# Kernel optimization log

Hardware: AMD Instinct MI355X
Metric: run time of the kernel (lower is better)

The kernel has to match this reference:

```python
import jax, jax.numpy as jnp
import numpy as np

MUL_IN = 32      # multiplicity of input 0e irrep (input channels)
MUL_OUT = 32     # multiplicity of each output irrep
NUM_RB = 8       # num_radial_basis
DIAMETER = 5.0
STEPS = (1.0, 1.0, 1.0)
GRID = 32
BATCH = 2
OUT_DIM = MUL_OUT * (1 + 3 + 5)  # 32x0e + 32x1o + 32x2e = 288


def _sus(x):
    # smooth unit step used by e3nn's 'smooth_finite' basis
    return jnp.where(x > 0.0, jnp.exp(-1.0 / jnp.where(x > 0.0, x, 1.0)), 0.0)


def _soft_one_hot(x, start, end, number):
    # e3nn.soft_one_hot_linspace, basis='smooth_finite', start_zero=end_zero=True
    values = jnp.linspace(start, end, number + 2)
    step = values[1] - values[0]
    values = values[1:-1]
    d = (x[..., None] - values) / step
    return 1.14136 * jnp.exp(2.0) * _sus(d + 1.0) * _sus(1.0 - d)


def _lattice():
    r = DIAMETER / 2
    axes = []
    for st in STEPS:
        s = int(np.floor(r / st))
        axes.append(jnp.arange(-s, s + 1.0, dtype=jnp.float32) * st)
    return jnp.stack(jnp.meshgrid(*axes, indexing='ij'), axis=-1)  # [X,Y,Z,3]


def _sph(lattice):
    # e3nn real spherical harmonics (component normalization, normalize=True),
    # e3nn axis/order convention: l=1 -> (y, z, x)
    n = jnp.linalg.norm(lattice, axis=-1, keepdims=True)
    u = lattice / jnp.where(n == 0.0, 1.0, n)
    x, y, z = u[..., 0], u[..., 1], u[..., 2]
    y0 = jnp.ones_like(x)[..., None]
    y1 = jnp.sqrt(3.0) * jnp.stack([y, z, x], axis=-1)
    y2 = jnp.stack([
        jnp.sqrt(15.0) * x * y,
        jnp.sqrt(15.0) * y * z,
        (jnp.sqrt(5.0) / 2.0) * (2.0 * z**2 - x**2 - y**2),
        jnp.sqrt(15.0) * x * z,
        (jnp.sqrt(15.0) / 2.0) * (x**2 - y**2),
    ], axis=-1)
    return [y0, y1, y2]


def _kernel(w0, w1, w2, w_lin):
    lat = _lattice()
    nvox = lat.shape[0] * lat.shape[1] * lat.shape[2]
    emb = _soft_one_hot(jnp.linalg.norm(lat, axis=-1), 0.0, DIAMETER / 2, NUM_RB)
    ys = _sph(lat)
    fan = jnp.sqrt(jnp.asarray(MUL_IN, emb.dtype))  # fully-connected TP path norm
    blocks = []
    for w, y in zip((w0, w1, w2), ys):
        # radial weights per (in-mul u, out-mul v): [X,Y,Z,u,v]
        W = jnp.einsum('xyzk,kuv->xyzuv', emb, w) / nvox
        # scalar-input TP path 0e x l -> l reduces to outer product with Y_lm
        blk = jnp.einsum('xyzuv,xyzm->xyzuvm', W, y) / fan
        blocks.append(blk.reshape(blk.shape[:4] + (-1,)))  # flatten (v, m)
    k = jnp.concatenate(blocks, axis=-1)  # [X,Y,Z,MUL_IN,OUT_DIM]
    # self-connection (FunctionalLinear) replaces the center tap; only 0e->0e path
    center = jnp.concatenate(
        [w_lin / fan, jnp.zeros((MUL_IN, MUL_OUT * (3 + 5)), k.dtype)], axis=-1)
    cx, cy, cz = k.shape[0] // 2, k.shape[1] // 2, k.shape[2] // 2
    return k.at[cx, cy, cz].set(center)


def setup_inputs() -> dict:
    key = jax.random.key(0)
    ks = jax.random.split(key, 5)
    return {
        'x': jax.random.normal(ks[0], (BATCH, GRID, GRID, GRID, MUL_IN), jnp.float32),
        'w0': jax.random.normal(ks[1], (NUM_RB, MUL_IN, MUL_OUT), jnp.float32),
        'w1': jax.random.normal(ks[2], (NUM_RB, MUL_IN, MUL_OUT), jnp.float32),
        'w2': jax.random.normal(ks[3], (NUM_RB, MUL_IN, MUL_OUT), jnp.float32),
        'w_lin': jax.random.normal(ks[4], (MUL_IN, MUL_OUT), jnp.float32),
    }


def reference(x, w0, w1, w2, w_lin):
    k = _kernel(w0, w1, w2, w_lin)  # [5,5,5,32,288]
    return jax.lax.conv_general_dilated(
        x, k, window_strides=(1, 1, 1), padding='SAME',
        dimension_numbers=('NXYZC', 'XYZIO', 'NXYZC'))
```

## Files before the change

### kernel.cpp

```cpp
#include <hip/hip_runtime.h>

typedef __bf16 bf16x8 __attribute__((ext_vector_type(8)));
typedef float f32x4 __attribute__((ext_vector_type(4)));

#define KT_BYTES 2304000
#define NS 18432

__device__ __forceinline__ unsigned short f2bf(float f) {
    unsigned int u = __builtin_bit_cast(unsigned int, f);
    unsigned int r = (u + 0x7fffu + ((u >> 16) & 1u)) >> 16;
    return (unsigned short)r;
}

__device__ __forceinline__ float sus(float x) {
    return x > 0.0f ? expf(-1.0f / x) : 0.0f;
}

struct VoxTab { int kt[81]; int xb[81]; };
constexpr VoxTab mk_tab() {
    VoxTab t{};
    int n = 0;
    for (int dx = 0; dx < 5; dx++)
        for (int dy = 0; dy < 5; dy++)
            for (int dz = 0; dz < 5; dz++) {
                int a = dx - 2, b = dy - 2, c = dz - 2;
                if (a * a + b * b + c * c <= 6) {
                    t.kt[n] = (dx * 25 + dy * 5 + dz) * NS;
                    t.xb[n] = ((dx * 36 + dy) * 36 + dz) * 32;
                    n++;
                }
            }
    return t;
}
__constant__ VoxTab TAB = mk_tab();

__global__ __launch_bounds__(512) void build_kt(const float* __restrict__ w0,
                                                const float* __restrict__ w1,
                                                const float* __restrict__ w2,
                                                const float* __restrict__ wlin,
                                                unsigned short* __restrict__ kt) {
    __shared__ float lw[24576];
    const int tid = threadIdx.x;
    {
        const float4* s0 = (const float4*)w0;
        const float4* s1 = (const float4*)w1;
        const float4* s2 = (const float4*)w2;
        for (int u = tid; u < 6144; u += 512) {
            int wsel = u >> 11, r = u & 2047;
            float4 v = (wsel == 0 ? s0[r] : (wsel == 1 ? s1[r] : s2[r]));
            ((float4*)lw)[u] = v;
        }
    }
    __syncthreads();

    const int v = blockIdx.x;
    const int dx = v / 25, dy = (v / 5) % 5, dz = v % 5;
    const float lx = (float)(dx - 2), ly = (float)(dy - 2), lz = (float)(dz - 2);
    const float nr = sqrtf(lx * lx + ly * ly + lz * lz);

    float emb[8];
    const float tt = nr * (9.0f / 2.5f);
    const float C = 1.14136f * expf(2.0f);
    #pragma unroll
    for (int j = 1; j <= 8; j++) {
        float d = tt - (float)j;
        emb[j - 1] = C * sus(d + 1.0f) * sus(1.0f - d);
    }

    float ux = 0.f, uy = 0.f, uz = 0.f;
    if (nr > 0.0f) { ux = lx / nr; uy = ly / nr; uz = lz / nr; }
    float Y[9];
    const float s3 = 1.7320508075688772f, s15 = 3.872983346207417f;
    Y[0] = 1.0f;
    Y[1] = s3 * uy; Y[2] = s3 * uz; Y[3] = s3 * ux;
    Y[4] = s15 * ux * uy;
    Y[5] = s15 * uy * uz;
    Y[6] = 1.1180339887498949f * (2.0f * uz * uz - ux * ux - uy * uy);
    Y[7] = s15 * ux * uz;
    Y[8] = 0.5f * s15 * (ux * ux - uy * uy);

    const float rfan = 0.17677669529663687f;

    for (int e = tid; e < 9216; e += 512) {
        const int ci = e / 288, o = e % 288;
        int wsel, co, yi;
        if (o < 32)       { wsel = 0; co = o; yi = 0; }
        else if (o < 128) { int t = o - 32;  wsel = 1; co = t / 3; yi = 1 + t % 3; }
        else              { int t = o - 128; wsel = 2; co = t / 5; yi = 4 + t % 5; }
        const float* w = lw + wsel * 8192;
        float s = 0.0f;
        #pragma unroll
        for (int k = 0; k < 8; k++) s += emb[k] * w[k * 1024 + ci * 32 + co];
        float val = s * (1.0f / 125.0f) * Y[yi] * rfan;
        if (v == 62) val = (o < 32) ? wlin[ci * 32 + o] * rfan : 0.0f;
        int r = o * 64 + ci * 2;
        int rs = r ^ (((r >> 7) & 7) << 4);
        kt[v * 9216 + (rs >> 1)] = f2bf(val);
    }
}

__global__ void pad_x2(const float* __restrict__ x, unsigned short* __restrict__ xb) {
    int u = blockIdx.x * blockDim.x + threadIdx.x;
    if (u >= 373248) return;
    const int ci8 = u & 3;
    int t = u >> 2;
    const int pz = t % 36; t /= 36;
    const int py = t % 36; t /= 36;
    const int px = t % 36; const int nn = t / 36;
    const int gx = px - 2, gy = py - 2, gz = pz - 2;
    uint4 ov = {0u, 0u, 0u, 0u};
    if ((unsigned)gx < 32u && (unsigned)gy < 32u && (unsigned)gz < 32u) {
        const float* src = x + ((((size_t)nn * 32 + gx) * 32 + gy) * 32 + gz) * 32 + ci8 * 8;
        float4 f0 = ((const float4*)src)[0];
        float4 f1 = ((const float4*)src)[1];
        ov.x = (unsigned)f2bf(f0.x) | ((unsigned)f2bf(f0.y) << 16);
        ov.y = (unsigned)f2bf(f0.z) | ((unsigned)f2bf(f0.w) << 16);
        ov.z = (unsigned)f2bf(f1.x) | ((unsigned)f2bf(f1.y) << 16);
        ov.w = (unsigned)f2bf(f1.z) | ((unsigned)f2bf(f1.w) << 16);
    }
    ((uint4*)xb)[u] = ov;
}

__global__ __launch_bounds__(512, 2) void conv_mfma(const unsigned short* __restrict__ xb,
                                                    const unsigned short* __restrict__ kt,
                                                    float* __restrict__ out) {
    __shared__ __align__(16) char lds[3 * NS];
    const int tid = threadIdx.x;
    const int lane = tid & 63;
    const int wv = tid >> 6;
    const int l15 = lane & 15, l16 = lane >> 4;
    const int wm = wv & 3, wn = wv >> 2;
    const int o0 = wn * 144;

    const int b = blockIdx.x;
    const int sw = (b & 7) * 32 + (b >> 3);
    const int nn = sw >> 7;
    const int X0 = 2 * ((sw >> 3) & 15);
    const int Y0 = 4 * (sw & 7);

    const unsigned short* xbase = xb + (size_t)nn * 1492992;

    int aoff[4];
    #pragma unroll
    for (int s = 0; s < 4; s++) {
        int xw = X0 + (wm >> 1);
        int yw = Y0 + (wm & 1) * 2 + (s >> 1);
        int zb = (s & 1) * 16 + l15;
        aoff[s] = ((xw * 36 + yw) * 36 + zb) * 32 + l16 * 8;
    }
    int boff[9];
    #pragma unroll
    for (int nt = 0; nt < 9; nt++) {
        int a = (o0 + nt * 16 + l15) * 64 + l16 * 16;
        boff[nt] = a ^ (((a >> 7) & 7) << 4);
    }

    auto stageB = [&](int ktByte, int slot) {
        const char* src = (const char*)kt + ktByte + wv * 2304;
        char* dst = lds + slot * NS + wv * 2304;
        __builtin_amdgcn_global_load_lds(
            (const __attribute__((address_space(1))) void*)(src + lane * 16),
            (__attribute__((address_space(3))) void*)dst, 16, 0, 0);
        __builtin_amdgcn_global_load_lds(
            (const __attribute__((address_space(1))) void*)(src + 1024 + lane * 16),
            (__attribute__((address_space(3))) void*)(dst + 1024), 16, 0, 0);
        __builtin_amdgcn_global_load_lds(
            (const __attribute__((address_space(1))) void*)(src + 2048 + lane * 4),
            (__attribute__((address_space(3))) void*)(dst + 2048), 4, 0, 0);
    };

    bf16x8 Ac[4], An[4];
    f32x4 acc[4][9];
    #pragma unroll
    for (int i = 0; i < 4; i++)
        #pragma unroll
        for (int j = 0; j < 9; j++)
            acc[i][j] = (f32x4){0.f, 0.f, 0.f, 0.f};

    auto loadA = [&](bf16x8* A, int xoff) {
        #pragma unroll
        for (int s = 0; s < 4; s++)
            A[s] = *(const bf16x8*)(xbase + aoff[s] + xoff);
    };

    auto issue = [&](int ktN, int slot2, int xbN) {
        if (ktN >= 0) stageB(ktN, slot2);
        if (xbN >= 0) loadA(An, xbN);
    };

    auto compute = [&](int slot) {
        #pragma unroll
        for (int nt = 0; nt < 9; nt++) {
            bf16x8 bfr = *(const bf16x8*)(lds + slot * NS + boff[nt]);
            #pragma unroll
            for (int s = 0; s < 4; s++)
                acc[s][nt] = __builtin_amdgcn_mfma_f32_16x16x32_bf16(Ac[s], bfr, acc[s][nt], 0, 0, 0);
        }
        __builtin_amdgcn_sched_barrier(0);
        __builtin_amdgcn_s_barrier();
        #pragma unroll
        for (int s = 0; s < 4; s++) Ac[s] = An[s];
    };

    stageB(TAB.kt[0], 0);
    loadA(Ac, TAB.xb[0]);
    stageB(TAB.kt[1], 1);
    asm volatile("s_waitcnt vmcnt(3)" ::: "memory");
    __builtin_amdgcn_sched_barrier(0);
    __builtin_amdgcn_s_barrier();

    #pragma unroll 1
    for (int g = 0; g < 26; g++) {
        const int k = g * 3;
        issue(TAB.kt[k + 2], 2, TAB.xb[k + 1]);
        asm volatile("s_waitcnt vmcnt(7)" ::: "memory");
        compute(0);
        issue(TAB.kt[k + 3], 0, TAB.xb[k + 2]);
        asm volatile("s_waitcnt vmcnt(7)" ::: "memory");
        compute(1);
        issue(TAB.kt[k + 4], 1, TAB.xb[k + 3]);
        asm volatile("s_waitcnt vmcnt(7)" ::: "memory");
        compute(2);
    }
    issue(TAB.kt[80], 2, TAB.xb[79]);
    asm volatile("s_waitcnt vmcnt(7)" ::: "memory");
    compute(0);
    issue(-1, 0, TAB.xb[80]);
    asm volatile("s_waitcnt vmcnt(4)" ::: "memory");
    compute(1);
    issue(-1, 0, -1);
    asm volatile("s_waitcnt vmcnt(0)" ::: "memory");
    compute(2);

    #pragma unroll
    for (int s = 0; s < 4; s++) {
        const int x = X0 + (wm >> 1);
        const int y = Y0 + (wm & 1) * 2 + (s >> 1);
        #pragma unroll
        for (int r = 0; r < 4; r++) {
            int z = (s & 1) * 16 + l16 * 4 + r;
            size_t base = ((((size_t)nn * 32 + x) * 32 + y) * 32 + z) * 288 + o0 + l15;
            #pragma unroll
            for (int nt = 0; nt < 9; nt++)
                out[base + nt * 16] = acc[s][nt][r];
        }
    }
}

extern "C" void kernel_launch(void* const* d_in, const int* in_sizes, int n_in,
                              void* d_out, int out_size, void* d_ws, size_t ws_size,
                              hipStream_t stream) {
    const float* x    = (const float*)d_in[0];
    const float* w0   = (const float*)d_in[1];
    const float* w1   = (const float*)d_in[2];
    const float* w2   = (const float*)d_in[3];
    const float* wlin = (const float*)d_in[4];
    unsigned short* kt = (unsigned short*)d_ws;
    unsigned short* xb = (unsigned short*)((char*)d_ws + KT_BYTES);
    float* out = (float*)d_out;

    hipLaunchKernelGGL(build_kt, dim3(125), dim3(512), 0, stream, w0, w1, w2, wlin, kt);
    hipLaunchKernelGGL(pad_x2, dim3(1458), dim3(256), 0, stream, x, xb);
    hipLaunchKernelGGL(conv_mfma, dim3(256), dim3(512), 0, stream, xb, kt, out);
}
```

Baseline: 129.3 us.

## Deepen kernel-tap prefetch to a 4-slot LDS ring with one barrier per phase

The MFMA convolution's LDS weight ring grows from three to four slots, so weight tiles are staged three taps ahead instead of two. The A-fragment registers now alternate between two named buffers rather than being copied each step. Each phase now waits once and synchronises with a single barrier before issuing the next loads, which simplifies the main loop. The tap table is padded from 81 to 87 entries with offset 0, which points at a corner kernel voxel that should be zero, so the padded steps add 3 wasted MFMA phases. The larger LDS footprint still has to fit two blocks per CU.

```diff
diff --git a/kernel.cpp b/kernel.cpp
--- a/kernel.cpp
+++ b/kernel.cpp
@@ -5,6 +5,7 @@
 
 #define KT_BYTES 2304000
 #define NS 18432
+#define NV 87
 
 __device__ __forceinline__ unsigned short f2bf(float f) {
     unsigned int u = __builtin_bit_cast(unsigned int, f);
@@ -16,7 +17,7 @@
     return x > 0.0f ? expf(-1.0f / x) : 0.0f;
 }
 
-struct VoxTab { int kt[81]; int xb[81]; };
+struct VoxTab { int kt[NV]; int xb[NV]; };
 constexpr VoxTab mk_tab() {
     VoxTab t{};
     int n = 0;
@@ -30,6 +31,7 @@
                     n++;
                 }
             }
+    for (; n < NV; n++) { t.kt[n] = 0; t.xb[n] = 0; }
     return t;
 }
 __constant__ VoxTab TAB = mk_tab();
@@ -124,7 +126,7 @@
 __global__ __launch_bounds__(512, 2) void conv_mfma(const unsigned short* __restrict__ xb,
                                                     const unsigned short* __restrict__ kt,
                                                     float* __restrict__ out) {
-    __shared__ __align__(16) char lds[3 * NS];
+    __shared__ __align__(16) char lds[4 * NS];
     const int tid = threadIdx.x;
     const int lane = tid & 63;
     const int wv = tid >> 6;
@@ -169,7 +171,7 @@
             (__attribute__((address_space(3))) void*)(dst + 2048), 4, 0, 0);
     };
 
-    bf16x8 Ac[4], An[4];
+    bf16x8 A0[4], A1[4];
     f32x4 acc[4][9];
     #pragma unroll
     for (int i = 0; i < 4; i++)
@@ -183,54 +185,39 @@
             A[s] = *(const bf16x8*)(xbase + aoff[s] + xoff);
     };
 
-    auto issue = [&](int ktN, int slot2, int xbN) {
-        if (ktN >= 0) stageB(ktN, slot2);
-        if (xbN >= 0) loadA(An, xbN);
-    };
-
-    auto compute = [&](int slot) {
+    auto compute = [&](bf16x8* A, int slot) {
         #pragma unroll
         for (int nt = 0; nt < 9; nt++) {
             bf16x8 bfr = *(const bf16x8*)(lds + slot * NS + boff[nt]);
             #pragma unroll
             for (int s = 0; s < 4; s++)
-                acc[s][nt] = __builtin_amdgcn_mfma_f32_16x16x32_bf16(Ac[s], bfr, acc[s][nt], 0, 0, 0);
+                acc[s][nt] = __builtin_amdgcn_mfma_f32_16x16x32_bf16(A[s], bfr, acc[s][nt], 0, 0, 0);
         }
-        __builtin_amdgcn_sched_barrier(0);
-        __builtin_amdgcn_s_barrier();
-        #pragma unroll
-        for (int s = 0; s < 4; s++) Ac[s] = An[s];
     };
 
+    #define PHASE(CUR, NXT, K)                                          \
+        asm volatile("s_waitcnt vmcnt(7)" ::: "memory");                \
+        __builtin_amdgcn_sched_barrier(0);                              \
+        __builtin_amdgcn_s_barrier();                                   \
+        __builtin_amdgcn_sched_barrier(0);                              \
+        stageB(TAB.kt[(K) + 3], ((K) + 3) & 3);                         \
+        loadA(NXT, TAB.xb[(K) + 1]);                                    \
+        compute(CUR, (K) & 3);
+
     stageB(TAB.kt[0], 0);
-    loadA(Ac, TAB.xb[0]);
     stageB(TAB.kt[1], 1);
-    asm volatile("s_waitcnt vmcnt(3)" ::: "memory");
-    __builtin_amdgcn_sched_barrier(0);
-    __builtin_amdgcn_s_barrier();
+    stageB(TAB.kt[2], 2);
+    loadA(A0, TAB.xb[0]);
 
     #pragma unroll 1
-    for (int g = 0; g < 26; g++) {
-        const int k = g * 3;
-        issue(TAB.kt[k + 2], 2, TAB.xb[k + 1]);
-        asm volatile("s_waitcnt vmcnt(7)" ::: "memory");
-        compute(0);
-        issue(TAB.kt[k + 3], 0, TAB.xb[k + 2]);
-        asm volatile("s_waitcnt vmcnt(7)" ::: "memory");
-        compute(1);
-        issue(TAB.kt[k + 4], 1, TAB.xb[k + 3]);
-        asm volatile("s_waitcnt vmcnt(7)" ::: "memory");
-        compute(2);
-    }
-    issue(TAB.kt[80], 2, TAB.xb[79]);
-    asm volatile("s_waitcnt vmcnt(7)" ::: "memory");
-    compute(0);
-    issue(-1, 0, TAB.xb[80]);
-    asm volatile("s_waitcnt vmcnt(4)" ::: "memory");
-    compute(1);
-    issue(-1, 0, -1);
-    asm volatile("s_waitcnt vmcnt(0)" ::: "memory");
-    compute(2);
+    for (int g = 0; g < 21; g++) {
+        const int k = g * 4;
+        PHASE(A0, A1, k + 0)
+        PHASE(A1, A0, k + 1)
+        PHASE(A0, A1, k + 2)
+        PHASE(A1, A0, k + 3)
+    }
+    #undef PHASE
 
     #pragma unroll
     for (int s = 0; s < 4; s++) {
```

New measurement: 130.8 us. No clear change (+1.2%).
